# Kernel tuning notes

Hardware: AMD Instinct MI355X
Metric: run time of the kernel (lower is better)

The kernel has to match this reference:

```python
import jax, jax.numpy as jnp
import numpy as np

NUM_CLASSES = 80
MASK_SIZE = 3
ATTRIBS = 5 + NUM_CLASSES
NET_W = 608.0
NET_H = 608.0
# Faithful to the original indexing bug: anchor_w = masked_anchors[a], anchor_h = masked_anchors[a+1]
MASKED_ANCHORS = np.array([10.0, 13.0, 16.0, 30.0, 33.0, 23.0], dtype=np.float32)
ANCHOR_W = jnp.asarray(MASKED_ANCHORS[0:MASK_SIZE])      # [10, 13, 16]
ANCHOR_H = jnp.asarray(MASKED_ANCHORS[1:MASK_SIZE + 1])  # [13, 16, 30]


def setup_inputs() -> dict:
    key = jax.random.key(0)
    x = jax.random.normal(key, (16, MASK_SIZE * ATTRIBS, 76, 76), dtype=jnp.float32)
    return {"x": x}


def reference(x):
    B, C, H, W = x.shape
    # (B, A, attribs, H, W) -> (B, A, H, W, attribs)
    pred = x.reshape(B, MASK_SIZE, ATTRIBS, H, W).transpose(0, 1, 3, 4, 2)
    tx = jax.nn.sigmoid(pred[..., 0])
    ty = jax.nn.sigmoid(pred[..., 1])
    tw = pred[..., 2]
    th = pred[..., 3]
    conf = jax.nn.sigmoid(pred[..., 4])
    pred_cls = jax.nn.sigmoid(pred[..., 5:])

    gi = jnp.arange(W, dtype=x.dtype)[None, None, None, :]  # column index i
    gj = jnp.arange(H, dtype=x.dtype)[None, None, :, None]  # row index j
    bx = (gi + tx) / W
    by = (gj + ty) / H
    bw = jnp.exp(tw) * ANCHOR_W[None, :, None, None] / NET_W
    bh = jnp.exp(th) * ANCHOR_H[None, :, None, None] / NET_H

    boxes = jnp.stack([bx, by, bw, bh], axis=-1)  # (B, A, H, W, 4)
    # (B, A, H, W, 4+1+num_classes)
    return jnp.concatenate([boxes, conf[..., None], pred_cls], axis=-1)
```

## Files before the change

kernel.cpp:

```cpp
#include <hip/hip_runtime.h>
#include <stdint.h>

#define NB       16
#define NA       3
#define HH_      76
#define WW_      76
#define S_TOT    (HH_ * WW_)
#define ATTR     85
#define TILE_S   76
#define TILES    (S_TOT / TILE_S)
#define NTHREADS 512
#define NWAVES   (NTHREADS / 64)
#define TW       (ATTR * TILE_S)
#define NSTG     ((TW + 63) / 64)
#define NSTGW    ((NSTG + NWAVES - 1) / NWAVES)
#define LDSW     (NSTG * 64)
#define UNITS2   (TW / 4)
#define NB2      4
#define LOG2E    1.44269504088896340f

typedef __attribute__((ext_vector_type(4))) float float4v;

__device__ __forceinline__ float fast_sigmoid(float x) {
    float e = __builtin_amdgcn_exp2f(x * (-LOG2E));
    return __builtin_amdgcn_rcpf(1.0f + e);
}

__global__ __launch_bounds__(NTHREADS, 8)
void yolo_layer_kernel(const float* __restrict__ in,
                       float* __restrict__ out) {
    __shared__ __attribute__((aligned(16))) float lds[LDSW];

    const int tid  = threadIdx.x;
    const int lane = tid & 63;
    const int wv   = tid >> 6;
    const int tile = blockIdx.x;
    const int BA   = blockIdx.y;
    const int a    = BA % NA;
    const int s0   = tile * TILE_S;

    const float aw = (a == 0) ? 10.0f : (a == 1) ? 13.0f : 16.0f;
    const float ah = (a == 0) ? 13.0f : (a == 1) ? 16.0f : 30.0f;
    const float cw = aw * (1.0f / 608.0f);
    const float ch = ah * (1.0f / 608.0f);

    const float* inb = in + (size_t)BA * (ATTR * S_TOT) + s0;

    #pragma unroll
    for (int i = 0; i < NSTGW; ++i) {
        int j = wv + i * NWAVES;
        if (j < NSTG) {
            int p  = j * 64 + lane;
            int pc = (p < TW) ? p : (TW - 1);
            int k  = pc / 76;
            int t  = pc - k * 76;
            int s  = t - (k >> 2);
            if (s < 0) s += 76;
            const float* g = inb + (size_t)k * S_TOT + s;
            __builtin_amdgcn_global_load_lds(
                (const __attribute__((address_space(1))) void*)g,
                (__attribute__((address_space(3))) void*)&lds[j * 64],
                4, 0, 0);
        }
    }
    __syncthreads();

    float4v* outv = (float4v*)(out + ((size_t)BA * S_TOT + s0) * ATTR);

    #pragma unroll
    for (int i = 0; i < NB2; ++i) {
        int u = tid + i * NTHREADS;
        if (u >= UNITS2) break;

        float r[4];
        #pragma unroll
        for (int e = 0; e < 4; ++e) {
            int idx = 4 * u + e;
            int s   = idx / 85;
            int k   = idx - s * 85;
            int t   = s + (k >> 2);
            if (t >= 76) t -= 76;
            float x = lds[k * 76 + t];

            if (k >= 4) {
                r[e] = fast_sigmoid(x);
            } else if (k == 0) {
                r[e] = ((float)s + fast_sigmoid(x)) * (1.0f / 76.0f);
            } else if (k == 1) {
                r[e] = ((float)tile + fast_sigmoid(x)) * (1.0f / 76.0f);
            } else {
                float ex = __builtin_amdgcn_exp2f(x * LOG2E);
                r[e] = ex * ((k == 2) ? cw : ch);
            }
        }

        float4v w = { r[0], r[1], r[2], r[3] };
        outv[u] = w;
    }
}

extern "C" void kernel_launch(void* const* d_in, const int* in_sizes, int n_in,
                              void* d_out, int out_size, void* d_ws, size_t ws_size,
                              hipStream_t stream) {
    const float* in = (const float*)d_in[0];
    float* out = (float*)d_out;

    dim3 grid(TILES, NB * NA);
    dim3 block(NTHREADS);
    yolo_layer_kernel<<<grid, block, 0, stream>>>(in, out);
}
```

Before: 167.0 us.

## Use persistent blocks with double-buffered 16-byte LDS staging of row tiles

Replaces the one-block-per-row grid with 512 persistent blocks, each looping over 7-8 row tiles. The next tile is prefetched into a second LDS buffer while the current one is computed. Staging now uses 16-byte global_load_lds into a rows-padded-to-96 rotated layout instead of 4-byte loads. exp(t) is derived as the reciprocal of the sigmoid's exp(-x), so every element needs a single exp. The aim is to hide load latency and cut staging instruction count, at the cost of more LDS per block, lower occupancy, and rcp precision differences for the box width and height.

```diff
diff --git a/kernel.cpp b/kernel.cpp
--- a/kernel.cpp
+++ b/kernel.cpp
@@ -8,94 +8,112 @@
 #define S_TOT    (HH_ * WW_)
 #define ATTR     85
 #define TILE_S   76
-#define TILES    (S_TOT / TILE_S)
+#define NTILES   (NB * NA * HH_)
+#define NBLK     512
 #define NTHREADS 512
-#define NWAVES   (NTHREADS / 64)
-#define TW       (ATTR * TILE_S)
-#define NSTG     ((TW + 63) / 64)
-#define NSTGW    ((NSTG + NWAVES - 1) / NWAVES)
-#define LDSW     (NSTG * 64)
-#define UNITS2   (TW / 4)
-#define NB2      4
+#define ROWP     96
+#define BUFW     8192
+#define NSTGW    4
+#define TW4      1615
 #define LOG2E    1.44269504088896340f
 
 typedef __attribute__((ext_vector_type(4))) float float4v;
 
-__device__ __forceinline__ float fast_sigmoid(float x) {
-    float e = __builtin_amdgcn_exp2f(x * (-LOG2E));
-    return __builtin_amdgcn_rcpf(1.0f + e);
-}
-
-__global__ __launch_bounds__(NTHREADS, 8)
+__global__ __launch_bounds__(NTHREADS, 4)
 void yolo_layer_kernel(const float* __restrict__ in,
                        float* __restrict__ out) {
-    __shared__ __attribute__((aligned(16))) float lds[LDSW];
+    __shared__ __attribute__((aligned(16))) float lds[2 * BUFW];
 
     const int tid  = threadIdx.x;
     const int lane = tid & 63;
     const int wv   = tid >> 6;
-    const int tile = blockIdx.x;
-    const int BA   = blockIdx.y;
-    const int a    = BA % NA;
-    const int s0   = tile * TILE_S;
+    const int b    = blockIdx.x;
 
-    const float aw = (a == 0) ? 10.0f : (a == 1) ? 13.0f : 16.0f;
-    const float ah = (a == 0) ? 13.0f : (a == 1) ? 16.0f : 30.0f;
-    const float cw = aw * (1.0f / 608.0f);
-    const float ch = ah * (1.0f / 608.0f);
-
-    const float* inb = in + (size_t)BA * (ATTR * S_TOT) + s0;
-
-    #pragma unroll
-    for (int i = 0; i < NSTGW; ++i) {
-        int j = wv + i * NWAVES;
-        if (j < NSTG) {
-            int p  = j * 64 + lane;
-            int pc = (p < TW) ? p : (TW - 1);
-            int k  = pc / 76;
-            int t  = pc - k * 76;
-            int s  = t - (k >> 2);
-            if (s < 0) s += 76;
-            const float* g = inb + (size_t)k * S_TOT + s;
+    auto STAGE = [&](int bufw, int lin) {
+        int tBA = lin / 76;
+        int ttr = lin - 76 * tBA;
+        const float* binb = in + (size_t)tBA * (ATTR * S_TOT) + ttr * WW_;
+        #pragma unroll
+        for (int ii = 0; ii < NSTGW; ++ii) {
+            int j  = (wv << 2) + ii;
+            int p  = (j << 8) + (lane << 2);
+            int k  = p / 96;
+            int t0 = p - 96 * k;
+            int kc = (k > 84) ? 84 : k;
+            int rot = (kc >> 2) << 2;
+            int tr = t0 - rot;
+            tr += (tr < 0) ? 96 : 0;
+            int ts = (tr <= 72) ? tr : 72;
+            if (k > 84) ts = 72;
+            const float* g = binb + (size_t)kc * S_TOT + ts;
             __builtin_amdgcn_global_load_lds(
                 (const __attribute__((address_space(1))) void*)g,
-                (__attribute__((address_space(3))) void*)&lds[j * 64],
-                4, 0, 0);
+                (__attribute__((address_space(3))) void*)&lds[bufw + (j << 8)],
+                16, 0, 0);
         }
-    }
-    __syncthreads();
+    };
 
-    float4v* outv = (float4v*)(out + ((size_t)BA * S_TOT + s0) * ATTR);
+    auto COMPUTE = [&](int bufw, int lin) {
+        int tBA = lin / 76;
+        int ttr = lin - 76 * tBA;
+        int ta  = tBA - 3 * (tBA / 3);
+        float aw = (ta == 0) ? 10.0f : (ta == 1) ? 13.0f : 16.0f;
+        float ah = (ta == 0) ? 13.0f : (ta == 1) ? 16.0f : 30.0f;
+        float cw = aw * (1.0f / 608.0f);
+        float ch = ah * (1.0f / 608.0f);
+        float trf = (float)ttr;
+        const float* L = &lds[bufw];
+        float4v* outv = (float4v*)out + (size_t)lin * TW4;
+        #pragma unroll
+        for (int i = 0; i < 4; ++i) {
+            int u = tid + i * NTHREADS;
+            if (u >= TW4) break;
+            int idx0 = u << 2;
+            int s  = idx0 / 85;
+            int k0 = idx0 - 85 * s;
+            float r[4];
+            #pragma unroll
+            for (int e = 0; e < 4; ++e) {
+                int k    = k0 + e;
+                int w    = (k >= 85) ? 1 : 0;
+                int keff = k - 85 * w;
+                int seff = s + w;
+                int rot  = (keff >> 2) << 2;
+                int t    = seff + rot;
+                t -= (t >= 96) ? 96 : 0;
+                float x  = L[keff * 96 + t];
+                float E  = __builtin_amdgcn_exp2f(x * (-LOG2E));
+                float sg = __builtin_amdgcn_rcpf(1.0f + E);
+                float rv;
+                if (keff >= 4)      rv = sg;
+                else if (keff == 0) rv = ((float)seff + sg) * (1.0f / 76.0f);
+                else if (keff == 1) rv = (trf + sg) * (1.0f / 76.0f);
+                else rv = __builtin_amdgcn_rcpf(E) *
+                          ((keff == 2) ? cw : ch);
+                r[e] = rv;
+            }
+            float4v w4 = { r[0], r[1], r[2], r[3] };
+            outv[u] = w4;
+        }
+    };
 
-    #pragma unroll
-    for (int i = 0; i < NB2; ++i) {
-        int u = tid + i * NTHREADS;
-        if (u >= UNITS2) break;
-
-        float r[4];
-        #pragma unroll
-        for (int e = 0; e < 4; ++e) {
-            int idx = 4 * u + e;
-            int s   = idx / 85;
-            int k   = idx - s * 85;
-            int t   = s + (k >> 2);
-            if (t >= 76) t -= 76;
-            float x = lds[k * 76 + t];
-
-            if (k >= 4) {
-                r[e] = fast_sigmoid(x);
-            } else if (k == 0) {
-                r[e] = ((float)s + fast_sigmoid(x)) * (1.0f / 76.0f);
-            } else if (k == 1) {
-                r[e] = ((float)tile + fast_sigmoid(x)) * (1.0f / 76.0f);
-            } else {
-                float ex = __builtin_amdgcn_exp2f(x * LOG2E);
-                r[e] = ex * ((k == 2) ? cw : ch);
-            }
+    const int n = (b < NTILES - 7 * NBLK) ? 8 : 7;
+    STAGE(0, b);
+    for (int i = 0; ; ) {
+        int lin = b + i * NBLK;
+        if (i + 1 < n) {
+            STAGE(((i + 1) & 1) * BUFW, lin + NBLK);
+            asm volatile("s_waitcnt vmcnt(4)" ::: "memory");
+        } else {
+            asm volatile("s_waitcnt vmcnt(0)" ::: "memory");
         }
-
-        float4v w = { r[0], r[1], r[2], r[3] };
-        outv[u] = w;
+        __builtin_amdgcn_sched_barrier(0);
+        __builtin_amdgcn_s_barrier();
+        __builtin_amdgcn_sched_barrier(0);
+        COMPUTE((i & 1) * BUFW, lin);
+        if (++i >= n) break;
+        __builtin_amdgcn_sched_barrier(0);
+        __builtin_amdgcn_s_barrier();
     }
 }
 
@@ -105,7 +123,7 @@
     const float* in = (const float*)d_in[0];
     float* out = (float*)d_out;
 
-    dim3 grid(TILES, NB * NA);
+    dim3 grid(NBLK);
     dim3 block(NTHREADS);
     yolo_layer_kernel<<<grid, block, 0, stream>>>(in, out);
 }
```

Result: slower. 171.3 us, median of 2 (+2.6%).
